# Kernel tuning notes

Measured on AMD Instinct MI355X. Metric: run time of the kernel, lower is better.

## Reference

```python
import jax, jax.numpy as jnp
import numpy as np

IN_FEATURES = 8192
OUT_FEATURES = 8192
CODESZ = 8            # E8 lattice dimension per code index
CODEBOOK_SIZE = 65536 # 2^16-entry codebook (16-bit indices)
TOKENS = 32           # decode-style batch


def fwht(x):
    """Fast Walsh-Hadamard transform (Sylvester order) along the last axis.
    n must be a power of 2. Unnormalized (multiply by H_n)."""
    n = x.shape[-1]
    steps = int(np.log2(n))
    h = 1
    for _ in range(steps):
        y = x.reshape(*x.shape[:-1], n // (2 * h), 2, h)
        a = y[..., 0, :]
        b = y[..., 1, :]
        x = jnp.stack([a + b, a - b], axis=-2).reshape(*y.shape[:-3], n)
        h *= 2
    return x


def setup_inputs() -> dict:
    key = jax.random.key(0)
    k0, k1, k2, k3, k4 = jax.random.split(key, 5)
    x = jax.random.normal(k0, (TOKENS, IN_FEATURES), dtype=jnp.float32)
    # learned codebook: CODEBOOK_SIZE vectors of CODESZ entries (E8P-like lattice points)
    codebook_table = jax.random.normal(k1, (CODEBOOK_SIZE, CODESZ), dtype=jnp.float32) * 0.1
    # quantized weight indices: [out_features, in_features // codesz]
    Qidxs = jax.random.randint(k2, (OUT_FEATURES, IN_FEATURES // CODESZ), 0, CODEBOOK_SIZE, dtype=jnp.int32)
    # random sign vectors (incoherence processing)
    SU = (2.0 * jax.random.randint(k3, (IN_FEATURES,), 0, 2) - 1.0).astype(jnp.float32)
    SV = (2.0 * jax.random.randint(k4, (OUT_FEATURES,), 0, 2) - 1.0).astype(jnp.float32)
    Wscale = jnp.array(0.02, dtype=jnp.float32)
    return {"x": x, "codebook_table": codebook_table, "Qidxs": Qidxs,
            "SU": SU, "SV": SV, "Wscale": Wscale}


def reference(x, codebook_table, Qidxs, SU, SV, Wscale):
    n_in = x.shape[-1]
    n_out = SV.shape[0]
    # input incoherence: sign flip then orthonormal Hadamard rotation (matmul_hadUt)
    xh = fwht(x * SU) * (1.0 / jnp.sqrt(jnp.float32(n_in)))  # [T, n_in]
    # codebook dequantization: gather lattice vectors and lay out as [n_out, n_in]
    W = codebook_table[Qidxs].reshape(n_out, n_in)
    # quantized matmul in the rotated basis
    z = xh @ W.T  # [T, n_out]
    # output rotation (matmul_hadU) + sign/scale (SV absorbs Wscale in the torch code)
    out = fwht(z) * (1.0 / jnp.sqrt(jnp.float32(n_out))) * (SV * Wscale)
    return out
```

## Files before the change

### kernel.cpp

```cpp
#include <hip/hip_runtime.h>
#include <hip/hip_bf16.h>


typedef __attribute__((ext_vector_type(16))) float f32x16;
typedef __attribute__((ext_vector_type(8))) __bf16 bf16x8;
typedef __attribute__((ext_vector_type(4))) __bf16 bf16x4;
typedef __attribute__((ext_vector_type(4))) int i32x4;

#define IN_F 8192
#define OUT_F 8192
#define TOKENS 32
#define KSPLIT 8
#define KCHUNK 1024
#define CH (KCHUNK / 8)
#define GROUPS (KCHUNK / 32)
#define DG 5
#define DI 7
#define INV_SQRT_8192 0.011048543456039806f
#define PAD(i) ((i) + ((i) >> 5))

#if __has_builtin(__builtin_amdgcn_raw_buffer_load_b128) && \
    __has_builtin(__builtin_amdgcn_make_buffer_rsrc)
#define HAVE_BUF 1
#else
#define HAVE_BUF 0
#endif

__device__ inline void h4_reg(float v[4]) {
    float t0 = v[0] + v[1], t1 = v[0] - v[1];
    float t2 = v[2] + v[3], t3 = v[2] - v[3];
    v[0] = t0 + t2; v[1] = t1 + t3; v[2] = t0 - t2; v[3] = t1 - t3;
}

__device__ inline void fwht1024(float v[4], float* st, int tid) {
    h4_reg(v);
    const int lane = tid & 63;
    #pragma unroll
    for (int m = 1; m < 64; m <<= 1) {
        #pragma unroll
        for (int j = 0; j < 4; ++j) {
            float p = __shfl_xor(v[j], m, 64);
            v[j] = (lane & m) ? (p - v[j]) : (v[j] + p);
        }
    }
    #pragma unroll
    for (int j = 0; j < 4; ++j) st[PAD(4 * tid + j)] = v[j];
    __syncthreads();
    #pragma unroll
    for (int j = 0; j < 4; ++j) v[j] = st[PAD(tid + j * 256)];
    h4_reg(v);
}

__global__ __launch_bounds__(256)
void prep_kernel(const float* __restrict__ cb, __bf16* __restrict__ cbb,
                 const float* __restrict__ x, const float* __restrict__ su,
                 __bf16* __restrict__ xh, float* __restrict__ z) {
    __shared__ float st[1056];
    const int tid = threadIdx.x;
    if (blockIdx.x < 512) {
        int i = blockIdx.x * 256 + tid;
        float4 vv = ((const float4*)cb)[i];
        bf16x4 o;
        o[0] = (__bf16)vv.x; o[1] = (__bf16)vv.y;
        o[2] = (__bf16)vv.z; o[3] = (__bf16)vv.w;
        ((bf16x4*)cbb)[i] = o;
        ((float2*)z)[i] = make_float2(0.f, 0.f);
        return;
    }
    const int id = blockIdx.x - 512;
    const int t = id >> 3, ch = id & 7;
    float sgn[8];
    #pragma unroll
    for (int k = 0; k < 8; ++k)
        sgn[k] = (__builtin_popcount(ch & k) & 1) ? -1.f : 1.f;
    float v[4] = {0.f, 0.f, 0.f, 0.f};
    #pragma unroll
    for (int k = 0; k < 8; ++k) {
        float4 xv = *(const float4*)(x + (size_t)t * IN_F + k * 1024 + tid * 4);
        float4 s4 = *(const float4*)(su + k * 1024 + tid * 4);
        v[0] += sgn[k] * xv.x * s4.x;
        v[1] += sgn[k] * xv.y * s4.y;
        v[2] += sgn[k] * xv.z * s4.z;
        v[3] += sgn[k] * xv.w * s4.w;
    }
    fwht1024(v, st, tid);
    __bf16* dst = xh + (size_t)t * IN_F + ch * 1024;
    #pragma unroll
    for (int j = 0; j < 4; ++j)
        dst[tid + j * 256] = (__bf16)(v[j] * INV_SQRT_8192);
}

__global__ __launch_bounds__(512, 4)
void qgemm_kernel(const int* __restrict__ qidxs,
                  const __bf16* __restrict__ cb,
                  const __bf16* __restrict__ xh,
                  float* __restrict__ z) {
    __shared__ __align__(16) __bf16 xt[TOKENS * KCHUNK];
    const int ks = blockIdx.x & (KSPLIT - 1);
    const int nb = blockIdx.x >> 3;
    const int tid = threadIdx.x;
    const int wave = tid >> 6, lane = tid & 63;
    const int h = lane >> 5, lc = lane & 31;
    const int n = nb * 256 + wave * 32 + lc;

    #pragma unroll
    for (int i = 0; i < 8; ++i) {
        int f = i * 512 + tid, r = f >> 7, c = f & 127;
        i32x4 v = *(const i32x4*)(xh + (size_t)r * IN_F + ks * KCHUNK + c * 8);
        *(i32x4*)(xt + ((r * CH + (c ^ (r & 7))) << 3)) = v;
    }
    __syncthreads();

    const int* qrow = qidxs + (size_t)n * (IN_F / 8) + ks * (KCHUNK / 8);

#if HAVE_BUF
    __amdgpu_buffer_rsrc_t rsrc = __builtin_amdgcn_make_buffer_rsrc(
        (void*)cb, (short)0, 65536 * 16, 0x00020000);
    #define GA(ix, au) __builtin_bit_cast(bf16x8, \
        __builtin_amdgcn_raw_buffer_load_b128(rsrc, (ix) << 4, 0, au))
#else
    const bf16x8* cbv = (const bf16x8*)cb;
    #define GA(ix, au) (cbv[ix])
#endif

    f32x16 acc;
    #pragma unroll
    for (int i = 0; i < 16; ++i) acc[i] = 0.f;

    i32x4 iv[GROUPS];
    bf16x8 bfr[GROUPS][2];

    #pragma unroll
    for (int g = 0; g < DI; ++g)
        iv[g] = *(const i32x4*)(qrow + g * 4);
    #pragma unroll
    for (int g = 0; g < DG; ++g) {
        if (g & 1) {
            bfr[g][0] = GA(h ? iv[g][1] : iv[g][0], 1);
            bfr[g][1] = GA(h ? iv[g][3] : iv[g][2], 1);
        } else {
            bfr[g][0] = GA(h ? iv[g][1] : iv[g][0], 0);
            bfr[g][1] = GA(h ? iv[g][3] : iv[g][2], 0);
        }
    }

    #pragma unroll
    for (int g = 0; g < GROUPS; ++g) {
        if (g + DI < GROUPS)
            iv[g + DI] = *(const i32x4*)(qrow + (g + DI) * 4);
        if (g + DG < GROUPS) {
            if ((g + DG) & 1) {
                bfr[g + DG][0] = GA(h ? iv[g + DG][1] : iv[g + DG][0], 1);
                bfr[g + DG][1] = GA(h ? iv[g + DG][3] : iv[g + DG][2], 1);
            } else {
                bfr[g + DG][0] = GA(h ? iv[g + DG][1] : iv[g + DG][0], 0);
                bfr[g + DG][1] = GA(h ? iv[g + DG][3] : iv[g + DG][2], 0);
            }
        }
        #pragma unroll
        for (int sgi = 0; sgi < 2; ++sgi) {
            const int T = 2 * g + sgi;
            bf16x8 a = *(const bf16x8*)(xt +
                          ((lc * CH + ((2 * T + h) ^ (lc & 7))) << 3));
            acc = __builtin_amdgcn_mfma_f32_32x32x16_bf16(a, bfr[g][sgi],
                                                          acc, 0, 0, 0);
        }
    }

    #pragma unroll
    for (int r = 0; r < 16; ++r) {
        int m = (r & 3) + 4 * h + 8 * (r >> 2);
        atomicAdd(z + (size_t)m * OUT_F + n, acc[r]);
    }
}

__global__ __launch_bounds__(256)
void zsum_kernel(const float* __restrict__ z, const float* __restrict__ sv,
                 const float* __restrict__ wscale, float* __restrict__ out) {
    __shared__ float st[1056];
    const int tid = threadIdx.x;
    const int t = blockIdx.x >> 3, ch = blockIdx.x & 7;
    float sgn[8];
    #pragma unroll
    for (int k = 0; k < 8; ++k)
        sgn[k] = (__builtin_popcount(ch & k) & 1) ? -1.f : 1.f;
    float v[4] = {0.f, 0.f, 0.f, 0.f};
    #pragma unroll
    for (int kk = 0; kk < 8; ++kk) {
        float4 zv = *(const float4*)(z + (size_t)t * OUT_F + kk * 1024 + tid * 4);
        v[0] += sgn[kk] * zv.x;
        v[1] += sgn[kk] * zv.y;
        v[2] += sgn[kk] * zv.z;
        v[3] += sgn[kk] * zv.w;
    }
    fwht1024(v, st, tid);
    const float sc = INV_SQRT_8192 * wscale[0];
    float* dst = out + (size_t)t * OUT_F + ch * 1024;
    const float* svp = sv + ch * 1024;
    #pragma unroll
    for (int j = 0; j < 4; ++j)
        dst[tid + j * 256] = v[j] * sc * svp[tid + j * 256];
}

extern "C" void kernel_launch(void* const* d_in, const int* in_sizes, int n_in,
                              void* d_out, int out_size, void* d_ws, size_t ws_size,
                              hipStream_t stream) {
    const float* x      = (const float*)d_in[0];
    const float* cb     = (const float*)d_in[1];
    const int*   qidxs  = (const int*)d_in[2];
    const float* su     = (const float*)d_in[3];
    const float* sv     = (const float*)d_in[4];
    const float* wscale = (const float*)d_in[5];
    float* out = (float*)d_out;

    char* ws = (char*)d_ws;
    __bf16* cbb = (__bf16*)ws;
    __bf16* xh  = (__bf16*)(ws + (1u << 20));
    float*  z   = (float*)(ws + (1u << 20) + (512u << 10));

    hipLaunchKernelGGL(prep_kernel, dim3(768), dim3(256), 0, stream,
                       cb, cbb, x, su, xh, z);
    hipLaunchKernelGGL(qgemm_kernel, dim3(32 * KSPLIT), dim3(512), 0, stream,
                       qidxs, cbb, xh, z);
    hipLaunchKernelGGL(zsum_kernel, dim3(256), dim3(256), 0, stream,
                       z, sv, wscale, out);
}
```

Before: 127.7 us.

## Route half of codebook gathers through global_load_lds with fixed-depth vmcnt pipeline

New measurement: 132.2 us. +3.5%, slower.

```diff
diff --git a/kernel.cpp b/kernel.cpp
--- a/kernel.cpp
+++ b/kernel.cpp
@@ -14,8 +14,8 @@
 #define KCHUNK 1024
 #define CH (KCHUNK / 8)
 #define GROUPS (KCHUNK / 32)
-#define DG 5
-#define DI 7
+#define DG 3
+#define DI 5
 #define INV_SQRT_8192 0.011048543456039806f
 #define PAD(i) ((i) + ((i) >> 5))
 
@@ -25,6 +25,14 @@
 #else
 #define HAVE_BUF 0
 #endif
+
+#if __has_builtin(__builtin_amdgcn_global_load_lds)
+#define HAVE_GLDS 1
+#else
+#define HAVE_GLDS 0
+#endif
+
+#define KEEP(x) asm volatile("" :: "v"(x))
 
 __device__ inline void h4_reg(float v[4]) {
     float t0 = v[0] + v[1], t1 = v[0] - v[1];
@@ -90,18 +98,20 @@
         dst[tid + j * 256] = (__bf16)(v[j] * INV_SQRT_8192);
 }
 
-__global__ __launch_bounds__(512, 4)
+__global__ __launch_bounds__(512, 2)
 void qgemm_kernel(const int* __restrict__ qidxs,
                   const __bf16* __restrict__ cb,
                   const __bf16* __restrict__ xh,
                   float* __restrict__ z) {
     __shared__ __align__(16) __bf16 xt[TOKENS * KCHUNK];
+    __shared__ __align__(16) char qs[8 * 4 * 1024];
     const int ks = blockIdx.x & (KSPLIT - 1);
     const int nb = blockIdx.x >> 3;
     const int tid = threadIdx.x;
     const int wave = tid >> 6, lane = tid & 63;
     const int h = lane >> 5, lc = lane & 31;
     const int n = nb * 256 + wave * 32 + lc;
+    char* qsw = qs + wave * 4096;
 
     #pragma unroll
     for (int i = 0; i < 8; ++i) {
@@ -123,46 +133,67 @@
     #define GA(ix, au) (cbv[ix])
 #endif
 
+#if HAVE_GLDS
+    #define GLDS(gp, lp) __builtin_amdgcn_global_load_lds( \
+        (const __attribute__((address_space(1))) unsigned int*)(gp), \
+        (__attribute__((address_space(3))) unsigned int*)(lp), 16, 0, 0)
+#endif
+
     f32x16 acc;
     #pragma unroll
     for (int i = 0; i < 16; ++i) acc[i] = 0.f;
 
     i32x4 iv[GROUPS];
-    bf16x8 bfr[GROUPS][2];
-
-    #pragma unroll
-    for (int g = 0; g < DI; ++g)
-        iv[g] = *(const i32x4*)(qrow + g * 4);
-    #pragma unroll
-    for (int g = 0; g < DG; ++g) {
-        if (g & 1) {
-            bfr[g][0] = GA(h ? iv[g][1] : iv[g][0], 1);
-            bfr[g][1] = GA(h ? iv[g][3] : iv[g][2], 1);
+    bf16x8 bfr0[GROUPS];
+#if !HAVE_GLDS
+    bf16x8 bfr1[GROUPS];
+#endif
+
+    #pragma unroll
+    for (int g = -DI; g < GROUPS; ++g) {
+        if (g + DI < GROUPS) {
+            iv[g + DI] = *(const i32x4*)(qrow + (g + DI) * 4);
         } else {
-            bfr[g][0] = GA(h ? iv[g][1] : iv[g][0], 0);
-            bfr[g][1] = GA(h ? iv[g][3] : iv[g][2], 0);
-        }
-    }
-
-    #pragma unroll
-    for (int g = 0; g < GROUPS; ++g) {
-        if (g + DI < GROUPS)
-            iv[g + DI] = *(const i32x4*)(qrow + (g + DI) * 4);
-        if (g + DG < GROUPS) {
-            if ((g + DG) & 1) {
-                bfr[g + DG][0] = GA(h ? iv[g + DG][1] : iv[g + DG][0], 1);
-                bfr[g + DG][1] = GA(h ? iv[g + DG][3] : iv[g + DG][2], 1);
+            i32x4 d = *(const i32x4*)qrow;
+            KEEP(d[0]);
+        }
+        if (g + DG >= 0) {
+            const int gg = g + DG;
+            if (gg < GROUPS) {
+                if (gg & 1) bfr0[gg] = GA(h ? iv[gg][1] : iv[gg][0], 1);
+                else        bfr0[gg] = GA(h ? iv[gg][1] : iv[gg][0], 0);
+                const unsigned ci = (unsigned)(h ? iv[gg][3] : iv[gg][2]);
+#if HAVE_GLDS
+                GLDS((const char*)cb + ((size_t)ci << 4),
+                     qsw + (gg & 3) * 1024);
+#else
+                if (gg & 1) bfr1[gg] = GA((int)ci, 1);
+                else        bfr1[gg] = GA((int)ci, 0);
+#endif
             } else {
-                bfr[g + DG][0] = GA(h ? iv[g + DG][1] : iv[g + DG][0], 0);
-                bfr[g + DG][1] = GA(h ? iv[g + DG][3] : iv[g + DG][2], 0);
+                bf16x8 d2 = GA(0, 0);
+                KEEP(__builtin_bit_cast(i32x4, d2)[0]);
+#if HAVE_GLDS
+                GLDS((const char*)cb, qsw + (gg & 3) * 1024);
+#endif
             }
         }
-        #pragma unroll
-        for (int sgi = 0; sgi < 2; ++sgi) {
-            const int T = 2 * g + sgi;
-            bf16x8 a = *(const bf16x8*)(xt +
-                          ((lc * CH + ((2 * T + h) ^ (lc & 7))) << 3));
-            acc = __builtin_amdgcn_mfma_f32_32x32x16_bf16(a, bfr[g][sgi],
+        if (g >= 0) {
+#if HAVE_GLDS
+            asm volatile("s_waitcnt vmcnt(9)" ::: "memory");
+            __builtin_amdgcn_sched_barrier(0);
+            bf16x8 b1 = *(const bf16x8*)(qsw + (g & 3) * 1024 + lane * 16);
+#else
+            bf16x8 b1 = bfr1[g];
+#endif
+            const int T0 = 2 * g, T1 = 2 * g + 1;
+            bf16x8 a0 = *(const bf16x8*)(xt +
+                          ((lc * CH + ((2 * T0 + h) ^ (lc & 7))) << 3));
+            acc = __builtin_amdgcn_mfma_f32_32x32x16_bf16(a0, bfr0[g],
+                                                          acc, 0, 0, 0);
+            bf16x8 a1 = *(const bf16x8*)(xt +
+                          ((lc * CH + ((2 * T1 + h) ^ (lc & 7))) << 3));
+            acc = __builtin_amdgcn_mfma_f32_32x32x16_bf16(a1, b1,
                                                           acc, 0, 0, 0);
         }
     }
```
